# Kernel optimization log

Hardware: AMD Instinct MI355X
Metric: run time of the kernel (lower is better)

## Reference

```python
import jax, jax.numpy as jnp
import numpy as np

# Sizes
NC, NT, NP = 100000, 300000, 50000   # customers, transactions, products
F, DIMC = 8, 16                      # columns per table, per-column embed dim
D = F * DIMC                         # 128 = proj_dim (lazy SAGEConv in-channels)
L, R = 2, 4                          # gnn layers, relation types
OUT = 10                             # out_channels
EM, EI = 300000, 600000              # edges: customer-makes-transaction, product-in-transaction


def setup_inputs() -> dict:
    key = jax.random.key(0)
    ks = jax.random.split(key, 14)
    s = 0.05
    return {
        "x_c": jax.random.normal(ks[0], (NC, F), jnp.float32),
        "x_t": jax.random.normal(ks[1], (NT, F), jnp.float32),
        "x_p": jax.random.normal(ks[2], (NP, F), jnp.float32),
        # per-table per-column numeric embedders: scalar -> DIMC (w*x + b)
        "W_col": jax.random.normal(ks[3], (3, F, DIMC), jnp.float32) * s,
        "b_col": jax.random.normal(ks[4], (3, F, DIMC), jnp.float32) * s,
        # SAGEConv weights per layer per relation: lin_l (neighbor) and lin_r (root)
        "Wn": jax.random.normal(ks[5], (L, R, D, D), jnp.float32) * s,
        "Wr": jax.random.normal(ks[6], (L, R, D, D), jnp.float32) * s,
        "b_lin": jax.random.normal(ks[7], (L, R, D), jnp.float32) * s,
        "W_out": jax.random.normal(ks[8], (D, OUT), jnp.float32) * s,
        "b_out": jax.random.normal(ks[9], (OUT,), jnp.float32) * s,
        "e_makes_src": jax.random.randint(ks[10], (EM,), 0, NC, jnp.int32),
        "e_makes_dst": jax.random.randint(ks[11], (EM,), 0, NT, jnp.int32),
        "e_in_src": jax.random.randint(ks[12], (EI,), 0, NP, jnp.int32),
        "e_in_dst": jax.random.randint(ks[13], (EI,), 0, NT, jnp.int32),
    }


def _embed(x, W, b):
    # x: [N, F]; W,b: [F, DIMC] -> [N, F*DIMC] (concat of per-column embeddings)
    n = x.shape[0]
    return (x[:, :, None] * W[None] + b[None]).reshape(n, -1)


def _sage(x_src, x_dst, src, dst, Wn, Wr, b, n_dst):
    # SAGEConv(mean): out = mean_neigh(x_src) @ Wn + b + x_dst @ Wr
    msg = jax.ops.segment_sum(x_src[src], dst, num_segments=n_dst)
    cnt = jax.ops.segment_sum(jnp.ones(src.shape[0], x_src.dtype), dst, num_segments=n_dst)
    mean = msg / jnp.maximum(cnt, 1.0)[:, None]  # isolated nodes -> 0 message
    return mean @ Wn + x_dst @ Wr + b


def reference(x_c, x_t, x_p, W_col, b_col, Wn, Wr, b_lin, W_out, b_out,
              e_makes_src, e_makes_dst, e_in_src, e_in_dst):
    h_c = _embed(x_c, W_col[0], b_col[0])
    h_t = _embed(x_t, W_col[1], b_col[1])
    h_p = _embed(x_p, W_col[2], b_col[2])
    for l in range(L):
        # R0: customer -makes-> transaction
        o_t0 = _sage(h_c, h_t, e_makes_src, e_makes_dst, Wn[l, 0], Wr[l, 0], b_lin[l, 0], NT)
        # R1: transaction -rev_makes-> customer
        o_c = _sage(h_t, h_c, e_makes_dst, e_makes_src, Wn[l, 1], Wr[l, 1], b_lin[l, 1], NC)
        # R2: product -in-> transaction
        o_t2 = _sage(h_p, h_t, e_in_src, e_in_dst, Wn[l, 2], Wr[l, 2], b_lin[l, 2], NT)
        # R3: transaction -rev_in-> product
        o_p = _sage(h_t, h_p, e_in_dst, e_in_src, Wn[l, 3], Wr[l, 3], b_lin[l, 3], NP)
        # HeteroConv(aggr='mean'): mean over relations targeting each dst type
        h_c, h_t, h_p = o_c, 0.5 * (o_t0 + o_t2), o_p
    logits = h_t @ W_out + b_out  # target_table = 'transaction'
    return jax.nn.softmax(logits, axis=1)
```

## Files before the change

### kernel.cpp

```cpp
#include <hip/hip_runtime.h>

#define NCV 100000
#define NTV 300000
#define NPV 50000
#define DD 128
#define OUTC 10
#define EMV 300000
#define EIV 600000
#define YST 16

__global__ __launch_bounds__(256) void prep_T_w(
    const float* __restrict__ Wn10, const float* __restrict__ Wn12,
    const float* __restrict__ Wr10, const float* __restrict__ Wr12,
    const float* __restrict__ Wout, float* __restrict__ T) {
  int gw = (blockIdx.x * 256 + threadIdx.x) >> 6;
  int lane = threadIdx.x & 63;
  if (gw >= 3 * 1280) return;
  int mat = gw / 1280, r = gw % 1280, n = r / 10, o = r % 10;
  float s = 0.f;
  #pragma unroll
  for (int mi = 0; mi < 2; ++mi) {
    int m = lane + mi * 64;
    float w;
    if (mat == 0) w = Wn10[n * 128 + m];
    else if (mat == 1) w = Wn12[n * 128 + m];
    else w = 0.5f * (Wr10[n * 128 + m] + Wr12[n * 128 + m]);
    s += w * Wout[m * 10 + o];
  }
  #pragma unroll
  for (int d = 32; d; d >>= 1) s += __shfl_xor(s, d);
  if (lane == 0) T[gw] = s;
}

__global__ __launch_bounds__(256) void prep_Q_w(
    const float* __restrict__ Wn01, const float* __restrict__ Wr01,
    const float* __restrict__ Wn03, const float* __restrict__ Wr03,
    const float* __restrict__ Wn00, const float* __restrict__ Wn02,
    const float* __restrict__ Wr00, const float* __restrict__ Wr02,
    const float* __restrict__ T, float* __restrict__ Q) {
  int gw = (blockIdx.x * 256 + threadIdx.x) >> 6;
  int lane = threadIdx.x & 63;
  if (gw >= 7 * 1280) return;
  int q = gw / 1280, r = gw % 1280, k = r / 10, o = r % 10;
  const float* T1 = T, *T2 = T + 1280, *T3 = T + 2560;
  float s = 0.f;
  #pragma unroll
  for (int ni = 0; ni < 2; ++ni) {
    int n = lane + ni * 64;
    float w, t;
    switch (q) {
      case 0: w = Wn01[k * 128 + n]; t = T1[n * 10 + o]; break;
      case 1: w = Wr01[k * 128 + n]; t = T1[n * 10 + o]; break;
      case 2: w = Wn03[k * 128 + n]; t = T2[n * 10 + o]; break;
      case 3: w = Wr03[k * 128 + n]; t = T2[n * 10 + o]; break;
      case 4: w = Wn00[k * 128 + n]; t = T3[n * 10 + o]; break;
      case 5: w = Wn02[k * 128 + n]; t = T3[n * 10 + o]; break;
      default: w = Wr00[k * 128 + n] + Wr02[k * 128 + n]; t = T3[n * 10 + o]; break;
    }
    s += w * t;
  }
  #pragma unroll
  for (int d = 32; d; d >>= 1) s += __shfl_xor(s, d);
  if (lane == 0) Q[gw] = s;
}

__global__ __launch_bounds__(256) void prep_B_w(
    const float* __restrict__ Wcol, const float* __restrict__ bcol,
    const float* __restrict__ b_lin, const float* __restrict__ Wout,
    const float* __restrict__ bout, const float* __restrict__ T,
    const float* __restrict__ Q, float* __restrict__ B) {
  int gw = (blockIdx.x * 256 + threadIdx.x) >> 6;
  int lane = threadIdx.x & 63;
  if (gw >= 450) return;
  int r = gw / 10, o = gw % 10;
  const float* WcC = Wcol, *WcT = Wcol + 128, *WcP = Wcol + 256;
  const float* bC = bcol, *bT = bcol + 128, *bP = bcol + 256;
  const float* Q1 = Q, *Q2 = Q + 1280, *Q3 = Q + 2560, *Q4 = Q + 3840;
  const float* Q5 = Q + 5120, *Q6 = Q + 6400, *Q7 = Q + 7680;
  const float* T1 = T, *T2 = T + 1280, *T3 = T + 2560;
  const float* b00 = b_lin, *b01 = b_lin + 128, *b02 = b_lin + 256, *b03 = b_lin + 384;
  const float* b10 = b_lin + 512, *b12 = b_lin + 768;
  float s = 0.f;
  if (r < 8) {
    if (lane < 16) s = WcT[r * 16 + lane] * Q1[(r * 16 + lane) * 10 + o];
  } else if (r < 16) {
    int j = r - 8;
    if (lane < 16)
      s = WcC[j * 16 + lane] * (Q2[(j * 16 + lane) * 10 + o] + Q5[(j * 16 + lane) * 10 + o]);
  } else if (r == 16) {
    for (int k2 = lane; k2 < 128; k2 += 64) s += bT[k2] * Q1[k2 * 10 + o];
  } else if (r < 25) {
    int j = r - 17;
    if (lane < 16) s = WcT[j * 16 + lane] * Q3[(j * 16 + lane) * 10 + o];
  } else if (r < 33) {
    int j = r - 25;
    if (lane < 16)
      s = WcP[j * 16 + lane] * (Q4[(j * 16 + lane) * 10 + o] + Q6[(j * 16 + lane) * 10 + o]);
  } else if (r == 33) {
    for (int k2 = lane; k2 < 128; k2 += 64) s += bT[k2] * Q3[k2 * 10 + o];
  } else if (r < 42) {
    int j = r - 34;
    if (lane < 16) s = WcT[j * 16 + lane] * Q7[(j * 16 + lane) * 10 + o];
  } else if (r == 42) {
    for (int k2 = lane; k2 < 128; k2 += 64)
      s += bC[k2] * (Q2[k2 * 10 + o] + Q5[k2 * 10 + o]) + b01[k2] * T1[k2 * 10 + o];
  } else if (r == 43) {
    for (int k2 = lane; k2 < 128; k2 += 64)
      s += bP[k2] * (Q4[k2 * 10 + o] + Q6[k2 * 10 + o]) + b03[k2] * T2[k2 * 10 + o];
  } else {
    for (int n = lane; n < 128; n += 64)
      s += (b10[n] + b12[n]) * Wout[n * 10 + o] + bT[n] * Q7[n * 10 + o] +
           (b00[n] + b02[n]) * T3[n * 10 + o];
  }
  #pragma unroll
  for (int d = 32; d; d >>= 1) s += __shfl_xor(s, d);
  if (lane == 0) {
    float v = s * 0.5f;
    if (r == 44) v += bout[o];
    B[gw] = v;
  }
}

__global__ __launch_bounds__(256) void build_graph(
    const int* __restrict__ ems, const int* __restrict__ emd,
    const int* __restrict__ eis, const int* __restrict__ eid,
    int* __restrict__ head_c, int* __restrict__ head_p,
    int* __restrict__ heads_t,
    int2* __restrict__ cn_m, int2* __restrict__ tn_m,
    int2* __restrict__ pn_i, int2* __restrict__ tn_i) {
  int e = blockIdx.x * 256 + threadIdx.x;
  if (e < EMV) {
    int c = ems[e], t = emd[e];
    int cn = atomicExch(&head_c[c], e);
    int tn = atomicExch(&heads_t[2 * t], e);
    cn_m[e] = make_int2(cn, t);
    tn_m[e] = make_int2(tn, c);
  }
  if (e < EIV) {
    int p = eis[e], t = eid[e];
    int pn = atomicExch(&head_p[p], e);
    int tn = atomicExch(&heads_t[2 * t + 1], e);
    pn_i[e] = make_int2(pn, t);
    tn_i[e] = make_int2(tn, p);
  }
}

__global__ __launch_bounds__(256) void gather_y(
    const float* __restrict__ xt,
    const int* __restrict__ head_c, const int* __restrict__ head_p,
    const int2* __restrict__ cn_m, const int2* __restrict__ pn_i,
    const float* __restrict__ xc, const float* __restrict__ xp,
    const float* __restrict__ B,
    float* __restrict__ y_c, float* __restrict__ y_p) {
  __shared__ float sB[340];
  int tid = threadIdx.x;
  for (int i = tid; i < 340; i += 256) sB[i] = B[i];
  __syncthreads();
  int i = blockIdx.x * 256 + tid;
  if (i >= NCV + NPV) return;
  bool isC = i < NCV;
  int idx = isC ? i : i - NCV;
  const int2* nodes = isC ? cn_m : pn_i;
  int e = isC ? head_c[idx] : head_p[idx];

  float acc[8] = {0.f, 0.f, 0.f, 0.f, 0.f, 0.f, 0.f, 0.f};
  float cnt = 0.f;
  while (e >= 0) {
    int2 v = nodes[e];
    const float4* xr = (const float4*)(xt + (size_t)v.y * 8);
    float4 u = xr[0], w = xr[1];
    acc[0] += u.x; acc[1] += u.y; acc[2] += u.z; acc[3] += u.w;
    acc[4] += w.x; acc[5] += w.y; acc[6] += w.z; acc[7] += w.w;
    cnt += 1.f;
    e = v.x;
  }

  const float* xo = (isC ? xc : xp) + (size_t)idx * 8;
  const float* Bs = sB + (isC ? 0 : 170);
  float gg = cnt > 0.f ? 1.f : 0.f;
  float inv = gg / fmaxf(cnt, 1.f);
  float lg[OUTC];
  #pragma unroll
  for (int o = 0; o < OUTC; ++o) lg[o] = gg * Bs[16 * 10 + o];
  #pragma unroll
  for (int r = 0; r < 8; ++r) {
    float zb = acc[r] * inv;
    float zo = xo[r];
    #pragma unroll
    for (int o = 0; o < OUTC; ++o)
      lg[o] += zb * Bs[r * 10 + o] + zo * Bs[(8 + r) * 10 + o];
  }
  float4* yv = (float4*)((isC ? y_c : y_p) + (size_t)idx * YST);
  yv[0] = make_float4(lg[0], lg[1], lg[2], lg[3]);
  yv[1] = make_float4(lg[4], lg[5], lg[6], lg[7]);
  yv[2] = make_float4(lg[8], lg[9], 0.f, 0.f);
  yv[3] = make_float4(0.f, 0.f, 0.f, 0.f);
}

__global__ __launch_bounds__(256) void gather_t(
    const float* __restrict__ y_c, const float* __restrict__ y_p,
    const float* __restrict__ xt,
    const int* __restrict__ heads_t,
    const int2* __restrict__ tn_m, const int2* __restrict__ tn_i,
    const float* __restrict__ B, float* __restrict__ out) {
  __shared__ float sB[110];
  int tid = threadIdx.x;
  for (int i = tid; i < 110; i += 256) sB[i] = B[340 + i];
  __syncthreads();
  int t = blockIdx.x * 256 + tid;
  if (t >= NTV) return;

  int2 ht = ((const int2*)heads_t)[t];
  int e1 = ht.x, e2 = ht.y;

  float sc[OUTC] = {0.f, 0.f, 0.f, 0.f, 0.f, 0.f, 0.f, 0.f, 0.f, 0.f};
  float sp[OUTC] = {0.f, 0.f, 0.f, 0.f, 0.f, 0.f, 0.f, 0.f, 0.f, 0.f};
  float dc = 0.f, dp = 0.f;
  while (e1 >= 0 || e2 >= 0) {
    if (e1 >= 0) {
      int2 v = tn_m[e1];
      const float* yr = y_c + (size_t)v.y * YST;
      float4 u = *(const float4*)yr;
      float4 w = *(const float4*)(yr + 4);
      float2 z = *(const float2*)(yr + 8);
      sc[0] += u.x; sc[1] += u.y; sc[2] += u.z; sc[3] += u.w;
      sc[4] += w.x; sc[5] += w.y; sc[6] += w.z; sc[7] += w.w;
      sc[8] += z.x; sc[9] += z.y;
      dc += 1.f;
      e1 = v.x;
    }
    if (e2 >= 0) {
      int2 v = tn_i[e2];
      const float* yr = y_p + (size_t)v.y * YST;
      float4 u = *(const float4*)yr;
      float4 w = *(const float4*)(yr + 4);
      float2 z = *(const float2*)(yr + 8);
      sp[0] += u.x; sp[1] += u.y; sp[2] += u.z; sp[3] += u.w;
      sp[4] += w.x; sp[5] += w.y; sp[6] += w.z; sp[7] += w.w;
      sp[8] += z.x; sp[9] += z.y;
      dp += 1.f;
      e2 = v.x;
    }
  }

  float Gc = dc > 0.f ? 1.f : 0.f, Gp = dp > 0.f ? 1.f : 0.f;
  float ivc = 1.f / fmaxf(dc, 1.f), ivp = 1.f / fmaxf(dp, 1.f);

  const float4* xp4 = (const float4*)(xt + (size_t)t * 8);
  float4 xa = xp4[0], xb = xp4[1];
  float xv[8] = {xa.x, xa.y, xa.z, xa.w, xb.x, xb.y, xb.z, xb.w};

  float lg[OUTC];
  #pragma unroll
  for (int o = 0; o < OUTC; ++o)
    lg[o] = sc[o] * ivc + sp[o] * ivp +
            Gc * sB[80 + o] + Gp * sB[90 + o] + sB[100 + o];
  #pragma unroll
  for (int r = 0; r < 8; ++r) {
    float xr = xv[r];
    #pragma unroll
    for (int o = 0; o < OUTC; ++o) lg[o] += xr * sB[r * 10 + o];
  }

  float m = lg[0];
  #pragma unroll
  for (int o = 1; o < OUTC; ++o) m = fmaxf(m, lg[o]);
  float s = 0.f;
  #pragma unroll
  for (int o = 0; o < OUTC; ++o) { lg[o] = __expf(lg[o] - m); s += lg[o]; }
  float invs = 1.0f / s;
  float* op = &out[(size_t)t * OUTC];
  #pragma unroll
  for (int o = 0; o < 5; ++o) {
    float2 p2; p2.x = lg[2 * o] * invs; p2.y = lg[2 * o + 1] * invs;
    *(float2*)&op[2 * o] = p2;
  }
}

extern "C" void kernel_launch(void* const* d_in, const int* in_sizes, int n_in,
                              void* d_out, int out_size, void* d_ws, size_t ws_size,
                              hipStream_t stream) {
  const float* x_c   = (const float*)d_in[0];
  const float* x_t   = (const float*)d_in[1];
  const float* x_p   = (const float*)d_in[2];
  const float* W_col = (const float*)d_in[3];
  const float* b_col = (const float*)d_in[4];
  const float* Wn    = (const float*)d_in[5];
  const float* Wr    = (const float*)d_in[6];
  const float* b_lin = (const float*)d_in[7];
  const float* W_out = (const float*)d_in[8];
  const float* b_out = (const float*)d_in[9];
  const int* e_m_src = (const int*)d_in[10];
  const int* e_m_dst = (const int*)d_in[11];
  const int* e_i_src = (const int*)d_in[12];
  const int* e_i_dst = (const int*)d_in[13];
  float* out = (float*)d_out;

  size_t cursor = 0;
  char* base = (char*)d_ws;
  auto alloc = [&](size_t bytes) {
    void* p = base + cursor;
    cursor += (bytes + 255) & ~(size_t)255;
    return p;
  };
  int nheads = NCV + NPV + 2 * NTV;
  int* heads   = (int*)alloc((size_t)nheads * 4);
  int* head_c  = heads;
  int* head_p  = heads + NCV;
  int* heads_t = heads + NCV + NPV;
  int2* cn_m = (int2*)alloc((size_t)EMV * 8);
  int2* tn_m = (int2*)alloc((size_t)EMV * 8);
  int2* pn_i = (int2*)alloc((size_t)EIV * 8);
  int2* tn_i = (int2*)alloc((size_t)EIV * 8);
  float* y_c = (float*)alloc((size_t)NCV * YST * 4);
  float* y_p = (float*)alloc((size_t)NPV * YST * 4);
  float* T   = (float*)alloc(3 * 1280 * 4);
  float* Q   = (float*)alloc(7 * 1280 * 4);
  float* B   = (float*)alloc(450 * 4);

  const float* Wn_l[2][4]; const float* Wr_l[2][4];
  for (int l = 0; l < 2; ++l)
    for (int r = 0; r < 4; ++r) {
      Wn_l[l][r] = Wn + (size_t)(l * 4 + r) * DD * DD;
      Wr_l[l][r] = Wr + (size_t)(l * 4 + r) * DD * DD;
    }

  hipMemsetAsync(heads, 0xFF, (size_t)nheads * 4, stream);

  build_graph<<<(EIV + 255) / 256, 256, 0, stream>>>(
      e_m_src, e_m_dst, e_i_src, e_i_dst,
      head_c, head_p, heads_t, cn_m, tn_m, pn_i, tn_i);

  prep_T_w<<<(3 * 1280 * 64 + 255) / 256, 256, 0, stream>>>(
      Wn_l[1][0], Wn_l[1][2], Wr_l[1][0], Wr_l[1][2], W_out, T);
  prep_Q_w<<<(7 * 1280 * 64 + 255) / 256, 256, 0, stream>>>(
      Wn_l[0][1], Wr_l[0][1], Wn_l[0][3], Wr_l[0][3],
      Wn_l[0][0], Wn_l[0][2], Wr_l[0][0], Wr_l[0][2], T, Q);
  prep_B_w<<<(450 * 64 + 255) / 256, 256, 0, stream>>>(
      W_col, b_col, b_lin, W_out, b_out, T, Q, B);

  gather_y<<<(NCV + NPV + 255) / 256, 256, 0, stream>>>(
      x_t, head_c, head_p, cn_m, pn_i, x_c, x_p, B, y_c, y_p);

  gather_t<<<(NTV + 255) / 256, 256, 0, stream>>>(
      y_c, y_p, x_t, heads_t, tn_m, tn_i, B, out);
}
```

Measured before the change: 236.5 us.

## Embed transaction features into linked-list nodes and fuse graph build with prep_T

The edge-list build now copies each destination transaction's 8 features into a 64-byte node record next to the next-pointer. The customer/product gather then walks the list without a dependent second load into x_t. The weight-precompute prep_T kernel is merged into the same launch as extra blocks, which removes one launch. In exchange the build writes much more memory (64 bytes per edge instead of 8) and does a random x_t read per edge at build time.

```diff
diff --git a/kernel.cpp b/kernel.cpp
--- a/kernel.cpp
+++ b/kernel.cpp
@@ -8,28 +8,73 @@
 #define EMV 300000
 #define EIV 600000
 #define YST 16
-
-__global__ __launch_bounds__(256) void prep_T_w(
+#define NHEADS (NCV + NPV + 2 * NTV)
+#define NEB ((EIV + 255) / 256)
+#define PTB ((3 * 1280 * 64) / 256)
+
+__device__ __forceinline__ float i2f(int v) { return __int_as_float(v); }
+
+__global__ __launch_bounds__(256) void build_fat_prepT(
+    const int* __restrict__ ems, const int* __restrict__ emd,
+    const int* __restrict__ eis, const int* __restrict__ eid,
+    const float* __restrict__ xt,
+    int* __restrict__ head_c, int* __restrict__ head_p,
+    int* __restrict__ heads_t,
+    int4* __restrict__ cnm, int4* __restrict__ cni,
+    int2* __restrict__ tn_m, int2* __restrict__ tn_i,
     const float* __restrict__ Wn10, const float* __restrict__ Wn12,
     const float* __restrict__ Wr10, const float* __restrict__ Wr12,
     const float* __restrict__ Wout, float* __restrict__ T) {
-  int gw = (blockIdx.x * 256 + threadIdx.x) >> 6;
-  int lane = threadIdx.x & 63;
-  if (gw >= 3 * 1280) return;
-  int mat = gw / 1280, r = gw % 1280, n = r / 10, o = r % 10;
-  float s = 0.f;
-  #pragma unroll
-  for (int mi = 0; mi < 2; ++mi) {
-    int m = lane + mi * 64;
-    float w;
-    if (mat == 0) w = Wn10[n * 128 + m];
-    else if (mat == 1) w = Wn12[n * 128 + m];
-    else w = 0.5f * (Wr10[n * 128 + m] + Wr12[n * 128 + m]);
-    s += w * Wout[m * 10 + o];
-  }
-  #pragma unroll
-  for (int d = 32; d; d >>= 1) s += __shfl_xor(s, d);
-  if (lane == 0) T[gw] = s;
+  int b = blockIdx.x;
+  int tid = threadIdx.x;
+  if (b < NEB) {
+    int e = b * 256 + tid;
+    int4 z = make_int4(0, 0, 0, 0);
+    if (e < EMV) {
+      int c = ems[e], t = emd[e];
+      int cn = atomicExch(&head_c[c], e);
+      int tn = atomicExch(&heads_t[2 * t], e);
+      const int4* xr = (const int4*)(xt + (size_t)t * 8);
+      int4 x0 = xr[0], x1 = xr[1];
+      size_t bb = 4 * (size_t)e;
+      cnm[bb]     = make_int4(cn, x0.x, x0.y, x0.z);
+      cnm[bb + 1] = make_int4(x0.w, x1.x, x1.y, x1.z);
+      cnm[bb + 2] = make_int4(x1.w, 0, 0, 0);
+      cnm[bb + 3] = z;
+      tn_m[e] = make_int2(tn, c);
+    }
+    if (e < EIV) {
+      int p = eis[e], t = eid[e];
+      int pn = atomicExch(&head_p[p], e);
+      int tn = atomicExch(&heads_t[2 * t + 1], e);
+      const int4* xr = (const int4*)(xt + (size_t)t * 8);
+      int4 x0 = xr[0], x1 = xr[1];
+      size_t bb = 4 * (size_t)e;
+      cni[bb]     = make_int4(pn, x0.x, x0.y, x0.z);
+      cni[bb + 1] = make_int4(x0.w, x1.x, x1.y, x1.z);
+      cni[bb + 2] = make_int4(x1.w, 0, 0, 0);
+      cni[bb + 3] = z;
+      tn_i[e] = make_int2(tn, p);
+    }
+  } else {
+    int gw = ((b - NEB) * 256 + tid) >> 6;
+    int lane = tid & 63;
+    if (gw >= 3 * 1280) return;
+    int mat = gw / 1280, r = gw % 1280, n = r / 10, o = r % 10;
+    float s = 0.f;
+    #pragma unroll
+    for (int mi = 0; mi < 2; ++mi) {
+      int m = lane + mi * 64;
+      float w;
+      if (mat == 0) w = Wn10[n * 128 + m];
+      else if (mat == 1) w = Wn12[n * 128 + m];
+      else w = 0.5f * (Wr10[n * 128 + m] + Wr12[n * 128 + m]);
+      s += w * Wout[m * 10 + o];
+    }
+    #pragma unroll
+    for (int d = 32; d; d >>= 1) s += __shfl_xor(s, d);
+    if (lane == 0) T[gw] = s;
+  }
 }
 
 __global__ __launch_bounds__(256) void prep_Q_w(
@@ -121,34 +166,9 @@
   }
 }
 
-__global__ __launch_bounds__(256) void build_graph(
-    const int* __restrict__ ems, const int* __restrict__ emd,
-    const int* __restrict__ eis, const int* __restrict__ eid,
-    int* __restrict__ head_c, int* __restrict__ head_p,
-    int* __restrict__ heads_t,
-    int2* __restrict__ cn_m, int2* __restrict__ tn_m,
-    int2* __restrict__ pn_i, int2* __restrict__ tn_i) {
-  int e = blockIdx.x * 256 + threadIdx.x;
-  if (e < EMV) {
-    int c = ems[e], t = emd[e];
-    int cn = atomicExch(&head_c[c], e);
-    int tn = atomicExch(&heads_t[2 * t], e);
-    cn_m[e] = make_int2(cn, t);
-    tn_m[e] = make_int2(tn, c);
-  }
-  if (e < EIV) {
-    int p = eis[e], t = eid[e];
-    int pn = atomicExch(&head_p[p], e);
-    int tn = atomicExch(&heads_t[2 * t + 1], e);
-    pn_i[e] = make_int2(pn, t);
-    tn_i[e] = make_int2(tn, p);
-  }
-}
-
 __global__ __launch_bounds__(256) void gather_y(
-    const float* __restrict__ xt,
     const int* __restrict__ head_c, const int* __restrict__ head_p,
-    const int2* __restrict__ cn_m, const int2* __restrict__ pn_i,
+    const int4* __restrict__ cnm, const int4* __restrict__ cni,
     const float* __restrict__ xc, const float* __restrict__ xp,
     const float* __restrict__ B,
     float* __restrict__ y_c, float* __restrict__ y_p) {
@@ -160,19 +180,21 @@
   if (i >= NCV + NPV) return;
   bool isC = i < NCV;
   int idx = isC ? i : i - NCV;
-  const int2* nodes = isC ? cn_m : pn_i;
+  const int4* cn = isC ? cnm : cni;
   int e = isC ? head_c[idx] : head_p[idx];
 
   float acc[8] = {0.f, 0.f, 0.f, 0.f, 0.f, 0.f, 0.f, 0.f};
   float cnt = 0.f;
   while (e >= 0) {
-    int2 v = nodes[e];
-    const float4* xr = (const float4*)(xt + (size_t)v.y * 8);
-    float4 u = xr[0], w = xr[1];
-    acc[0] += u.x; acc[1] += u.y; acc[2] += u.z; acc[3] += u.w;
-    acc[4] += w.x; acc[5] += w.y; acc[6] += w.z; acc[7] += w.w;
+    size_t b = 4 * (size_t)e;
+    int4 w0 = cn[b];
+    int4 w1 = cn[b + 1];
+    int4 w2 = cn[b + 2];
+    acc[0] += i2f(w0.y); acc[1] += i2f(w0.z); acc[2] += i2f(w0.w);
+    acc[3] += i2f(w1.x); acc[4] += i2f(w1.y); acc[5] += i2f(w1.z); acc[6] += i2f(w1.w);
+    acc[7] += i2f(w2.x);
     cnt += 1.f;
-    e = v.x;
+    e = w0.x;
   }
 
   const float* xo = (isC ? xc : xp) + (size_t)idx * 8;
@@ -303,14 +325,13 @@
     cursor += (bytes + 255) & ~(size_t)255;
     return p;
   };
-  int nheads = NCV + NPV + 2 * NTV;
-  int* heads   = (int*)alloc((size_t)nheads * 4);
+  int* heads   = (int*)alloc((size_t)NHEADS * 4);
   int* head_c  = heads;
   int* head_p  = heads + NCV;
   int* heads_t = heads + NCV + NPV;
-  int2* cn_m = (int2*)alloc((size_t)EMV * 8);
+  int4* cnm = (int4*)alloc((size_t)EMV * 64);
+  int4* cni = (int4*)alloc((size_t)EIV * 64);
   int2* tn_m = (int2*)alloc((size_t)EMV * 8);
-  int2* pn_i = (int2*)alloc((size_t)EIV * 8);
   int2* tn_i = (int2*)alloc((size_t)EIV * 8);
   float* y_c = (float*)alloc((size_t)NCV * YST * 4);
   float* y_p = (float*)alloc((size_t)NPV * YST * 4);
@@ -325,14 +346,13 @@
       Wr_l[l][r] = Wr + (size_t)(l * 4 + r) * DD * DD;
     }
 
-  hipMemsetAsync(heads, 0xFF, (size_t)nheads * 4, stream);
-
-  build_graph<<<(EIV + 255) / 256, 256, 0, stream>>>(
-      e_m_src, e_m_dst, e_i_src, e_i_dst,
-      head_c, head_p, heads_t, cn_m, tn_m, pn_i, tn_i);
-
-  prep_T_w<<<(3 * 1280 * 64 + 255) / 256, 256, 0, stream>>>(
+  hipMemsetAsync(heads, 0xFF, (size_t)NHEADS * 4, stream);
+
+  build_fat_prepT<<<NEB + PTB, 256, 0, stream>>>(
+      e_m_src, e_m_dst, e_i_src, e_i_dst, x_t,
+      head_c, head_p, heads_t, cnm, cni, tn_m, tn_i,
       Wn_l[1][0], Wn_l[1][2], Wr_l[1][0], Wr_l[1][2], W_out, T);
+
   prep_Q_w<<<(7 * 1280 * 64 + 255) / 256, 256, 0, stream>>>(
       Wn_l[0][1], Wr_l[0][1], Wn_l[0][3], Wr_l[0][3],
       Wn_l[0][0], Wn_l[0][2], Wr_l[0][0], Wr_l[0][2], T, Q);
@@ -340,7 +360,7 @@
       W_col, b_col, b_lin, W_out, b_out, T, Q, B);
 
   gather_y<<<(NCV + NPV + 255) / 256, 256, 0, stream>>>(
-      x_t, head_c, head_p, cn_m, pn_i, x_c, x_p, B, y_c, y_p);
+      head_c, head_p, cnm, cni, x_c, x_p, B, y_c, y_p);
 
   gather_t<<<(NTV + 255) / 256, 256, 0, stream>>>(
       y_c, y_p, x_t, heads_t, tn_m, tn_i, B, out);
```

After: 228.4 us. 3.4% less time.
